# Performance work log

Measured on AMD Instinct MI355X. Metric: run time of the kernel, lower is better.

The kernel has to match this reference:

```python
import jax, jax.numpy as jnp
import numpy as np

BIG = 1e10


def _cylinder_query(radius, hmin, hmax, nsample, xyz, new_xyz, rot):
    # xyz: (B,N,3), new_xyz: (B,P,3), rot: (B,P,3,3) -> idx: (B,P,nsample) int32
    diff = xyz[:, None, :, :] - new_xyz[:, :, None, :]          # (B,P,N,3)
    local = jnp.einsum('bpnc,bpcd->bpnd', diff, rot)            # (B,P,N,3)
    x, y, z = local[..., 0], local[..., 1], local[..., 2]
    r2 = y * y + z * z                                          # (B,P,N)
    in_cyl = (x >= hmin) & (x <= hmax) & (r2 < radius * radius)
    dist = jnp.where(in_cyl, r2, BIG)
    neg_vals, idx = jax.lax.top_k(-dist, nsample)               # smallest dists
    vals = -neg_vals
    valid = vals < 1e9
    first = idx[:, :, 0:1]
    idx = jnp.where(valid, idx, first)                          # (B,P,nsample)
    return idx


def _group(features, idx):
    # features: (B,C,N), idx: (B,P,S) -> (B,C,P,S)
    B, C, N = features.shape
    P, S = idx.shape[1], idx.shape[2]
    ft = jnp.swapaxes(features, 1, 2)                           # (B,N,C)
    flat = idx.reshape(B, P * S)
    out = jnp.take_along_axis(ft, flat[:, :, None], axis=1)     # (B,P*S,C)
    return jnp.transpose(out.reshape(B, P, S, C), (0, 3, 1, 2)) # (B,C,P,S)


def setup_inputs() -> dict:
    key = jax.random.key(0)
    k1, k2, k3, k4 = jax.random.split(key, 4)
    B, N, P, C = 4, 16384, 1024, 64
    xyz = jax.random.uniform(k1, (B, N, 3), dtype=jnp.float32)
    new_xyz = jax.random.uniform(k2, (B, P, 3), dtype=jnp.float32)
    rot = jax.random.normal(k3, (B, P, 3, 3), dtype=jnp.float32)
    features = jax.random.normal(k4, (B, C, N), dtype=jnp.float32)
    return {"radius": 0.3, "hmin": -0.02, "hmax": 0.04, "nsample": 32,
            "xyz": xyz, "new_xyz": new_xyz, "rot": rot, "features": features}


def reference(radius, hmin, hmax, nsample, xyz, new_xyz, rot, features):
    idx = _cylinder_query(radius, hmin, hmax, nsample, xyz, new_xyz, rot)
    xyz_t = jnp.swapaxes(xyz, 1, 2)                             # (B,3,N)
    grouped_xyz = _group(xyz_t, idx)                            # (B,3,P,S)
    grouped_xyz = grouped_xyz - jnp.swapaxes(new_xyz, 1, 2)[..., None]
    # rotate_xyz=True: (B,P,S,3) @ (B,P,3,3)
    g = jnp.transpose(grouped_xyz, (0, 2, 3, 1))
    g = jnp.einsum('bpsc,bpcd->bpsd', g, rot)
    grouped_xyz = jnp.transpose(g, (0, 3, 1, 2))                # (B,3,P,S)
    grouped_features = _group(features, idx)                    # (B,C,P,S)
    return jnp.concatenate([grouped_xyz, grouped_features], axis=1)
```

## Files before the change

kernel.cpp:

```cpp
#include <hip/hip_runtime.h>

#define CAP    4608
#define BIGK   1.0e300
#define IDXINF 0x7fffffff

__device__ __forceinline__ void cmpx(double& k, int& n, int lane, int stride, bool up) {
    double ok = __shfl_xor(k, stride);
    int    on = __shfl_xor(n, stride);
    bool oLess = (ok < k) || (ok == k && on < n);
    bool lower = (lane & stride) == 0;
    bool takeOther = lower ? (up ? oLess : !oLess) : (up ? !oLess : oLess);
    if (takeOther) { k = ok; n = on; }
}

__device__ __forceinline__ void wave_sort64(double& k, int& n, int lane, bool asc) {
    #pragma unroll
    for (int size = 2; size < 64; size <<= 1) {
        bool up = asc ? ((lane & size) == 0) : ((lane & size) != 0);
        #pragma unroll
        for (int stride = size >> 1; stride > 0; stride >>= 1)
            cmpx(k, n, lane, stride, up);
    }
    #pragma unroll
    for (int stride = 32; stride > 0; stride >>= 1)
        cmpx(k, n, lane, stride, asc);
}

__global__ __launch_bounds__(256) void select_kernel(
    const float* __restrict__ radius_p,
    const float* __restrict__ hmin_p,
    const float* __restrict__ hmax_p,
    const float* __restrict__ xyz,
    const float* __restrict__ new_xyz,
    const float* __restrict__ rot,
    float* __restrict__ out,
    unsigned short* __restrict__ selw)
{
    const int N = 16384, P = 1024, S = 32, OC = 67;
    const int bp  = blockIdx.x;
    const int b   = bp >> 10;
    const int p   = bp & (P - 1);
    const int tid = threadIdx.x;
    const int lane = tid & 63;
    const int wv   = tid >> 6;

    __shared__ unsigned short cn[CAP];
    __shared__ double wr2[256];
    __shared__ int    wn[256];
    __shared__ int    cnt;
    __shared__ int    cnt2;
    __shared__ int    sel[32];

    if (tid == 0) { cnt = 0; cnt2 = 0; }
    __syncthreads();

    const double radius = (double)radius_p[0];
    const double hmin   = (double)hmin_p[0];
    const double hmax   = (double)hmax_p[0];
    const double rad2   = radius * radius;

    const float* nx = new_xyz + (size_t)bp * 3;
    const double cx = nx[0], cy = nx[1], cz = nx[2];
    const float* rp = rot + (size_t)bp * 9;
    const double r00 = rp[0], r01 = rp[1], r02 = rp[2];
    const double r10 = rp[3], r11 = rp[4], r12 = rp[5];
    const double r20 = rp[6], r21 = rp[7], r22 = rp[8];

    const float cxf = (float)cx, cyf = (float)cy, czf = (float)cz;
    const float r00f = (float)r00, r01f = (float)r01, r02f = (float)r02;
    const float r10f = (float)r10, r11f = (float)r11, r12f = (float)r12;
    const float r20f = (float)r20, r21f = (float)r21, r22f = (float)r22;
    const float hminf = (float)hmin - 5.0e-4f;
    const float hmaxf = (float)hmax + 5.0e-4f;
    const float rad2f = (float)rad2 + 1.0e-3f;

    const float* xb = xyz + (size_t)b * N * 3;

    for (int it = 0; it < 16; ++it) {
        int g = it * 1024 + tid * 4;
        const float4* vp = reinterpret_cast<const float4*>(xb + (size_t)g * 3);
        float4 v0 = vp[0], v1 = vp[1], v2 = vp[2];
        float px[4], py[4], pz[4];
        px[0]=v0.x; py[0]=v0.y; pz[0]=v0.z;
        px[1]=v0.w; py[1]=v1.x; pz[1]=v1.y;
        px[2]=v1.z; py[2]=v1.w; pz[2]=v2.x;
        px[3]=v2.y; py[3]=v2.z; pz[3]=v2.w;
        #pragma unroll
        for (int k = 0; k < 4; ++k) {
            float dxf = px[k] - cxf, dyf = py[k] - cyf, dzf = pz[k] - czf;
            float xf  = fmaf(dxf, r00f, fmaf(dyf, r10f, dzf * r20f));
            float yf  = fmaf(dxf, r01f, fmaf(dyf, r11f, dzf * r21f));
            float zf  = fmaf(dxf, r02f, fmaf(dyf, r12f, dzf * r22f));
            float r2f = fmaf(yf, yf, zf * zf);
            if (xf >= hminf && xf <= hmaxf && r2f < rad2f) {
                int slot = atomicAdd(&cnt, 1);
                if (slot < CAP) cn[slot] = (unsigned short)(g + k);
            }
        }
    }
    __syncthreads();

    const int Mloose = min(cnt, CAP);

    double rk = BIGK; int rn = IDXINF;
    int msum = 0;
    const int nch = (Mloose + 63) >> 6;
    for (int ch = wv; ch < nch; ch += 4) {
        int j = (ch << 6) + lane;
        double ck = BIGK; int cnn = IDXINF;
        bool ok = false;
        if (j < Mloose) {
            int n = cn[j];
            double dx = (double)xb[n * 3 + 0] - cx;
            double dy = (double)xb[n * 3 + 1] - cy;
            double dz = (double)xb[n * 3 + 2] - cz;
            double x = dx * r00 + dy * r10 + dz * r20;
            double y = dx * r01 + dy * r11 + dz * r21;
            double z = dx * r02 + dy * r12 + dz * r22;
            double r2 = y * y + z * z;
            if (x >= hmin && x <= hmax && r2 < rad2) { ok = true; ck = r2; cnn = n; }
        }
        msum += __popcll(__ballot(ok));
        wave_sort64(ck, cnn, lane, false);
        if ((ck < rk) || (ck == rk && cnn < rn)) { rk = ck; rn = cnn; }
        #pragma unroll
        for (int stride = 32; stride > 0; stride >>= 1)
            cmpx(rk, rn, lane, stride, true);
    }
    if (lane == 0 && msum > 0) atomicAdd(&cnt2, msum);
    wr2[(wv << 6) + lane] = rk;
    wn [(wv << 6) + lane] = rn;
    __syncthreads();

    if (wv == 0) {
        const int Mtrue = cnt2;
        #pragma unroll
        for (int w = 1; w < 4; ++w) {
            int src = (w << 6) + (63 - lane);
            double ck = wr2[src]; int cnn = wn[src];
            if ((ck < rk) || (ck == rk && cnn < rn)) { rk = ck; rn = cnn; }
            #pragma unroll
            for (int stride = 32; stride > 0; stride >>= 1)
                cmpx(rk, rn, lane, stride, true);
        }
        int nsel  = min(Mtrue, S);
        int first = __shfl(rn, 0);
        int v = (lane < nsel) ? rn : ((nsel > 0) ? first : 0);
        if (lane < S) sel[lane] = v;
    }
    __syncthreads();

    if (tid < S) {
        int n = sel[tid];
        selw[(size_t)bp * S + tid] = (unsigned short)n;
        double dx = (double)xb[n * 3 + 0] - cx;
        double dy = (double)xb[n * 3 + 1] - cy;
        double dz = (double)xb[n * 3 + 2] - cz;
        float x = (float)(dx * r00 + dy * r10 + dz * r20);
        float y = (float)(dx * r01 + dy * r11 + dz * r21);
        float z = (float)(dx * r02 + dy * r12 + dz * r22);
        float* o = out + (((size_t)b * OC + 0) * P + p) * S + tid;
        o[0 * (size_t)P * S] = x;
        o[1 * (size_t)P * S] = y;
        o[2 * (size_t)P * S] = z;
    }
}

__global__ __launch_bounds__(256) void gather_kernel(
    const float* __restrict__ feat,
    const unsigned short* __restrict__ selw,
    float* __restrict__ out)
{
    const int N = 16384, P = 1024, C = 64, S = 32, OC = 67;
    const int bid  = blockIdx.x;
    const int c    = bid & 63;
    const int half = (bid >> 6) & 1;
    const int b    = bid >> 7;
    const int tid  = threadIdx.x;

    __shared__ unsigned short st[512 * 32];

    const uint4* sp = reinterpret_cast<const uint4*>(
        selw + ((size_t)b * P + half * 512) * S);
    uint4* dl = reinterpret_cast<uint4*>(st);
    #pragma unroll
    for (int k = 0; k < 8; ++k)
        dl[k * 256 + tid] = sp[k * 256 + tid];
    __syncthreads();

    const float* fr = feat + ((size_t)b * C + c) * N;
    float* ob = out + (((size_t)b * OC + 3 + c) * P + half * 512) * S;
    #pragma unroll 4
    for (int k = 0; k < 16; ++k) {
        int e4 = (k * 256 + tid) * 4;
        ushort4 ix = *reinterpret_cast<const ushort4*>(&st[e4]);
        float4 v;
        v.x = fr[ix.x]; v.y = fr[ix.y]; v.z = fr[ix.z]; v.w = fr[ix.w];
        *reinterpret_cast<float4*>(&ob[e4]) = v;
    }
}

extern "C" void kernel_launch(void* const* d_in, const int* in_sizes, int n_in,
                              void* d_out, int out_size, void* d_ws, size_t ws_size,
                              hipStream_t stream) {
    const float* radius  = (const float*)d_in[0];
    const float* hmin    = (const float*)d_in[1];
    const float* hmax    = (const float*)d_in[2];
    const float* xyz     = (const float*)d_in[4];
    const float* new_xyz = (const float*)d_in[5];
    const float* rot     = (const float*)d_in[6];
    const float* feat    = (const float*)d_in[7];
    float* out = (float*)d_out;
    unsigned short* selw = (unsigned short*)d_ws;

    hipLaunchKernelGGL(select_kernel, dim3(4096), dim3(256), 0, stream,
                       radius, hmin, hmax, xyz, new_xyz, rot, out, selw);
    hipLaunchKernelGGL(gather_kernel, dim3(512), dim3(256), 0, stream,
                       feat, selw, out);
}
```

Baseline: 122.8 us.

## Prefilter candidates by slab test only, prefetch next xyz chunk, scalarize gather

The coarse filter now tests only the axial coordinate using a precomputed projected center, which drops the y/z rotation and radial check from the per-point loop. The next xyz chunk is software-prefetched into registers while the current chunk is processed. The candidate cap grows to 8192, and on overflow the exact pass scans all N points instead of truncating. This fixes a possible correctness gap but admits more candidates into the double-precision sort stage and adds shared memory use. The gather loop also changes from ushort4/float4 vector accesses to scalar per-element accesses.

```diff
diff --git a/kernel.cpp b/kernel.cpp
--- a/kernel.cpp
+++ b/kernel.cpp
@@ -1,6 +1,6 @@
 #include <hip/hip_runtime.h>
 
-#define CAP    4608
+#define CAP    8192
 #define BIGK   1.0e300
 #define IDXINF 0x7fffffff
 
@@ -66,41 +66,40 @@
     const double r10 = rp[3], r11 = rp[4], r12 = rp[5];
     const double r20 = rp[6], r21 = rp[7], r22 = rp[8];
 
-    const float cxf = (float)cx, cyf = (float)cy, czf = (float)cz;
-    const float r00f = (float)r00, r01f = (float)r01, r02f = (float)r02;
-    const float r10f = (float)r10, r11f = (float)r11, r12f = (float)r12;
-    const float r20f = (float)r20, r21f = (float)r21, r22f = (float)r22;
+    const float r00f = (float)r00, r10f = (float)r10, r20f = (float)r20;
+    const float cpxf = (float)(cx * r00 + cy * r10 + cz * r20);
     const float hminf = (float)hmin - 5.0e-4f;
     const float hmaxf = (float)hmax + 5.0e-4f;
-    const float rad2f = (float)rad2 + 1.0e-3f;
 
     const float* xb = xyz + (size_t)b * N * 3;
-
+    const float4* vp = reinterpret_cast<const float4*>(xb);
+
+    float4 a0 = vp[tid * 3 + 0], a1 = vp[tid * 3 + 1], a2 = vp[tid * 3 + 2];
     for (int it = 0; it < 16; ++it) {
+        const float4* q = vp + ((it + 1) & 15) * 768 + tid * 3;
+        float4 b0 = q[0], b1 = q[1], b2 = q[2];
         int g = it * 1024 + tid * 4;
-        const float4* vp = reinterpret_cast<const float4*>(xb + (size_t)g * 3);
-        float4 v0 = vp[0], v1 = vp[1], v2 = vp[2];
         float px[4], py[4], pz[4];
-        px[0]=v0.x; py[0]=v0.y; pz[0]=v0.z;
-        px[1]=v0.w; py[1]=v1.x; pz[1]=v1.y;
-        px[2]=v1.z; py[2]=v1.w; pz[2]=v2.x;
-        px[3]=v2.y; py[3]=v2.z; pz[3]=v2.w;
+        px[0]=a0.x; py[0]=a0.y; pz[0]=a0.z;
+        px[1]=a0.w; py[1]=a1.x; pz[1]=a1.y;
+        px[2]=a1.z; py[2]=a1.w; pz[2]=a2.x;
+        px[3]=a2.y; py[3]=a2.z; pz[3]=a2.w;
         #pragma unroll
         for (int k = 0; k < 4; ++k) {
-            float dxf = px[k] - cxf, dyf = py[k] - cyf, dzf = pz[k] - czf;
-            float xf  = fmaf(dxf, r00f, fmaf(dyf, r10f, dzf * r20f));
-            float yf  = fmaf(dxf, r01f, fmaf(dyf, r11f, dzf * r21f));
-            float zf  = fmaf(dxf, r02f, fmaf(dyf, r12f, dzf * r22f));
-            float r2f = fmaf(yf, yf, zf * zf);
-            if (xf >= hminf && xf <= hmaxf && r2f < rad2f) {
+            float xf = fmaf(px[k], r00f, fmaf(py[k], r10f,
+                        fmaf(pz[k], r20f, -cpxf)));
+            if (xf >= hminf && xf <= hmaxf) {
                 int slot = atomicAdd(&cnt, 1);
                 if (slot < CAP) cn[slot] = (unsigned short)(g + k);
             }
         }
-    }
-    __syncthreads();
-
-    const int Mloose = min(cnt, CAP);
+        a0 = b0; a1 = b1; a2 = b2;
+    }
+    __syncthreads();
+
+    int  Mloose = cnt;
+    bool ident  = false;
+    if (Mloose > CAP) { Mloose = N; ident = true; }
 
     double rk = BIGK; int rn = IDXINF;
     int msum = 0;
@@ -110,7 +109,7 @@
         double ck = BIGK; int cnn = IDXINF;
         bool ok = false;
         if (j < Mloose) {
-            int n = cn[j];
+            int n = ident ? j : (int)cn[j];
             double dx = (double)xb[n * 3 + 0] - cx;
             double dy = (double)xb[n * 3 + 1] - cy;
             double dz = (double)xb[n * 3 + 2] - cz;
@@ -191,12 +190,9 @@
     const float* fr = feat + ((size_t)b * C + c) * N;
     float* ob = out + (((size_t)b * OC + 3 + c) * P + half * 512) * S;
     #pragma unroll 4
-    for (int k = 0; k < 16; ++k) {
-        int e4 = (k * 256 + tid) * 4;
-        ushort4 ix = *reinterpret_cast<const ushort4*>(&st[e4]);
-        float4 v;
-        v.x = fr[ix.x]; v.y = fr[ix.y]; v.z = fr[ix.z]; v.w = fr[ix.w];
-        *reinterpret_cast<float4*>(&ob[e4]) = v;
+    for (int k = 0; k < 64; ++k) {
+        int e = k * 256 + tid;
+        ob[e] = fr[st[e]];
     }
 }
 
```

Measured after the change: 230.4 us. +87.6%, slower.
